# Kernel tuning notes

Measured on AMD Instinct MI355X. Metric: run time of the kernel, lower is better.

## Reference

```python
import jax, jax.numpy as jnp
import numpy as np

N_MET = 200000
N_RXN = 400000
E_SUB = 800000
E_ALL = 1600000
HIDDEN = 64
MSG = 8
DT = 0.01
FRAME = 100
PERIOD = 1000.0
CIRC_AMP = 0.5
HOMEO = 0.1
BASELINE = 1.0


def setup_inputs() -> dict:
    key = jax.random.key(0)
    ks = jax.random.split(key, 12)
    x = jax.random.uniform(ks[0], (N_MET, 8), dtype=jnp.float32)
    met_sub = jax.random.randint(ks[1], (E_SUB,), 0, N_MET, dtype=jnp.int32)
    rxn_sub = jax.random.randint(ks[2], (E_SUB,), 0, N_RXN, dtype=jnp.int32)
    sto_sub = jax.random.uniform(ks[3], (E_SUB,), dtype=jnp.float32, minval=0.5, maxval=2.0)
    met_all = jax.random.randint(ks[4], (E_ALL,), 0, N_MET, dtype=jnp.int32)
    rxn_all = jax.random.randint(ks[5], (E_ALL,), 0, N_RXN, dtype=jnp.int32)
    sto_all = jax.random.normal(ks[6], (E_ALL,), dtype=jnp.float32)
    sub_w1 = jax.random.normal(ks[7], (2, HIDDEN), dtype=jnp.float32) / np.sqrt(2.0)
    sub_b1 = jnp.zeros((HIDDEN,), jnp.float32)
    sub_w2 = jax.random.normal(ks[8], (HIDDEN, MSG), dtype=jnp.float32) / np.sqrt(HIDDEN)
    sub_b2 = jnp.zeros((MSG,), jnp.float32)
    rate_w1 = jax.random.normal(ks[9], (MSG, HIDDEN), dtype=jnp.float32) / np.sqrt(MSG)
    rate_b1 = jnp.zeros((HIDDEN,), jnp.float32)
    rate_w2 = jax.random.normal(ks[10], (HIDDEN, 1), dtype=jnp.float32) / np.sqrt(HIDDEN)
    rate_b2 = jnp.zeros((1,), jnp.float32)
    log_k = jax.random.uniform(ks[11], (N_RXN,), dtype=jnp.float32, minval=-3.0, maxval=-1.0)
    return {"x": x, "met_sub": met_sub, "rxn_sub": rxn_sub, "sto_sub": sto_sub,
            "met_all": met_all, "rxn_all": rxn_all, "sto_all": sto_all,
            "sub_w1": sub_w1, "sub_b1": sub_b1, "sub_w2": sub_w2, "sub_b2": sub_b2,
            "rate_w1": rate_w1, "rate_b1": rate_b1, "rate_w2": rate_w2, "rate_b2": rate_b2,
            "log_k": log_k}


def reference(x, met_sub, rxn_sub, sto_sub, met_all, rxn_all, sto_all,
              sub_w1, sub_b1, sub_w2, sub_b2,
              rate_w1, rate_b1, rate_w2, rate_b2, log_k):
    conc = x[:, 3]                      # [N_MET]
    ext = x[:, 4] * 2.0                 # [N_MET]
    # per-substrate-edge message MLP: [E_SUB,2] -> [E_SUB,MSG]
    msg_in = jnp.stack([conc[met_sub], sto_sub], axis=-1)
    msg = jnp.tanh(msg_in @ sub_w1 + sub_b1) @ sub_w2 + sub_b2
    # scatter-add edge messages into reactions
    h_rxn = jax.ops.segment_sum(msg, rxn_sub, num_segments=N_RXN)  # [N_RXN, MSG]
    k = jnp.power(10.0, log_k)
    base_v = (jnp.tanh(h_rxn @ rate_w1 + rate_b1) @ rate_w2 + rate_b2)[:, 0]  # [N_RXN]
    # multiplicative_substrate modulation: mean external input over substrates
    n_sub = jnp.maximum(
        jax.ops.segment_sum(jnp.ones((E_SUB,), jnp.float32), rxn_sub, num_segments=N_RXN), 1.0)
    ext_mean = jax.ops.segment_sum(ext[met_sub], rxn_sub, num_segments=N_RXN) / n_sub
    v = k * ext_mean * base_v
    # flux limit (dt > 0): no substrate over-consumed in one step
    consumption = sto_sub * v[rxn_sub] * DT
    total = jax.ops.segment_sum(consumption, met_sub, num_segments=N_MET)
    active = total > 1e-12
    met_scale = jnp.where(active,
                          jnp.minimum(conc / jnp.where(active, total, 1.0), 1.0),
                          1.0)
    rxn_scale = jnp.minimum(
        jax.ops.segment_min(met_scale[met_sub], rxn_sub, num_segments=N_RXN), 1.0)
    v = v * rxn_scale
    # scatter stoichiometric contributions to metabolites
    contrib = sto_all * v[rxn_all]
    dxdt = jax.ops.segment_sum(contrib, met_all, num_segments=N_MET)
    # homeostatic relaxation with circadian-modulated constant baseline
    phase = 2.0 * np.pi * FRAME / PERIOD
    modulation = 1.0 + CIRC_AMP * np.sin(phase)
    c_target = BASELINE * modulation
    dxdt = dxdt - HOMEO * (conc - c_target)
    return dxdt[:, None]
```

## Files before the change

kernel.cpp:

```cpp
#include <hip/hip_runtime.h>

#define NMET 200000
#define NRXN 400000
#define ESUB 800000
#define EALL 1600000

#define NBB 196
#define EBA 8192
#define EBS 4096

#define NBUCK_M 391
#define NBUCK_R 782
#define MET_MASK 0x3FFFF
#define MCAP 1280

#define C_TARGET 1.29389262614623664f
#define DT_C 0.01f
#define HOMEO_C 0.1f
#define LOG2_10 3.32192809488736235f

__device__ __forceinline__ float fast_tanh(float x) {
    float e = __expf(2.0f * x);
    return 1.0f - 2.0f * __builtin_amdgcn_rcpf(e + 1.0f);
}

__global__ __launch_bounds__(512) void k_count_all(
    const int* __restrict__ met_all, const int* __restrict__ met_sub,
    const int* __restrict__ rxn_sub,
    int* __restrict__ blockHistA, int* __restrict__ blockHistS,
    int* __restrict__ blockHistR)
{
    __shared__ int hA[NBUCK_M];
    __shared__ int hS[NBUCK_M];
    __shared__ int hR[NBUCK_R];
    int t = threadIdx.x;
    for (int b = t; b < NBUCK_R; b += 512) hR[b] = 0;
    for (int b = t; b < NBUCK_M; b += 512) { hA[b] = 0; hS[b] = 0; }
    __syncthreads();
    int baseA = blockIdx.x * EBA;
    for (int i = t; i < EBA; i += 512) {
        int e = baseA + i;
        if (e < EALL) atomicAdd(&hA[met_all[e] >> 9], 1);
    }
    int baseS = blockIdx.x * EBS;
    for (int i = t; i < EBS; i += 512) {
        int e = baseS + i;
        if (e < ESUB) {
            atomicAdd(&hS[met_sub[e] >> 9], 1);
            atomicAdd(&hR[rxn_sub[e] >> 9], 1);
        }
    }
    __syncthreads();
    for (int b = t; b < NBUCK_M; b += 512) {
        blockHistA[(size_t)b * NBB + blockIdx.x] = hA[b];
        blockHistS[(size_t)b * NBB + blockIdx.x] = hS[b];
    }
    for (int b = t; b < NBUCK_R; b += 512)
        blockHistR[(size_t)b * NBB + blockIdx.x] = hR[b];
}

__global__ __launch_bounds__(256) void k_scan_all(
    int* __restrict__ blockHistA, int* __restrict__ blockHistS,
    int* __restrict__ blockHistR,
    int* __restrict__ btotalA, int* __restrict__ btotalS,
    int* __restrict__ btotalR)
{
    __shared__ int sc[256];
    int bid = blockIdx.x;
    int* row; int* tot;
    if (bid < NBUCK_M) { row = blockHistA + (size_t)bid * NBB; tot = btotalA + bid; }
    else if (bid < 2 * NBUCK_M) { row = blockHistS + (size_t)(bid - NBUCK_M) * NBB; tot = btotalS + (bid - NBUCK_M); }
    else { row = blockHistR + (size_t)(bid - 2 * NBUCK_M) * NBB; tot = btotalR + (bid - 2 * NBUCK_M); }
    int t = threadIdx.x;
    int val = (t < NBB) ? row[t] : 0;
    sc[t] = val;
    __syncthreads();
    for (int off = 1; off < 256; off <<= 1) {
        int add = (t >= off) ? sc[t - off] : 0;
        __syncthreads();
        sc[t] += add;
        __syncthreads();
    }
    if (t < NBB) row[t] = sc[t] - val;
    if (t == 255) *tot = sc[255];
}

__global__ __launch_bounds__(1024) void k_bstart3(
    const int* __restrict__ btotalA, int* __restrict__ startA,
    const int* __restrict__ btotalS, int* __restrict__ startS,
    const int* __restrict__ btotalR, int* __restrict__ startR)
{
    __shared__ int lds[1024];
    const int* tot; int* st; int nb;
    if (blockIdx.x == 0)      { tot = btotalA; st = startA; nb = NBUCK_M; }
    else if (blockIdx.x == 1) { tot = btotalS; st = startS; nb = NBUCK_M; }
    else                      { tot = btotalR; st = startR; nb = NBUCK_R; }
    int t = threadIdx.x;
    int val = (t < nb) ? tot[t] : 0;
    lds[t] = val;
    __syncthreads();
    for (int off = 1; off < 1024; off <<= 1) {
        int add = (t >= off) ? lds[t - off] : 0;
        __syncthreads();
        lds[t] += add;
        __syncthreads();
    }
    if (t < nb) st[t] = lds[t] - val;
    if (t == 1023) st[nb] = lds[1023];
}

__global__ __launch_bounds__(512) void k_rxn_scatter(
    const int* __restrict__ rxn_sub, const int* __restrict__ met_sub,
    const float* __restrict__ sto_sub,
    const int* __restrict__ blockHistR, const int* __restrict__ bucketStartR,
    uint2* __restrict__ recsR)
{
    __shared__ int cnt[NBUCK_R];
    __shared__ int loff[NBUCK_R];
    __shared__ int rnk[NBUCK_R];
    __shared__ int bbase[NBUCK_R];
    __shared__ unsigned short sbuck[EBS];
    __shared__ uint2 stage[EBS];
    __shared__ int sc[512];
    __shared__ int carry_s;
    int t = threadIdx.x;
    for (int b = t; b < NBUCK_R; b += 512) {
        cnt[b] = 0; rnk[b] = 0;
        bbase[b] = bucketStartR[b] + blockHistR[(size_t)b * NBB + blockIdx.x];
    }
    if (t == 0) carry_s = 0;
    __syncthreads();
    int base = blockIdx.x * EBS;
    int nrec = ESUB - base; if (nrec > EBS) nrec = EBS; if (nrec < 0) nrec = 0;

    for (int i = t; i < nrec; i += 512)
        atomicAdd(&cnt[rxn_sub[base + i] >> 9], 1);
    __syncthreads();
    for (int b0 = 0; b0 < NBUCK_R; b0 += 512) {
        int idx = b0 + t;
        int val = (idx < NBUCK_R) ? cnt[idx] : 0;
        sc[t] = val;
        __syncthreads();
        for (int off = 1; off < 512; off <<= 1) {
            int add = (t >= off) ? sc[t - off] : 0;
            __syncthreads();
            sc[t] += add;
            __syncthreads();
        }
        if (idx < NBUCK_R) loff[idx] = carry_s + sc[t] - val;
        __syncthreads();
        if (t == 511) carry_s += sc[511];
        __syncthreads();
    }
    for (int i = t; i < nrec; i += 512) {
        int e = base + i;
        int r = rxn_sub[e];
        int b = r >> 9;
        int pos = loff[b] + atomicAdd(&rnk[b], 1);
        uint2 rec;
        rec.x = (unsigned)(met_sub[e] | ((r & 511) << 18));
        rec.y = __float_as_uint(sto_sub[e]);
        stage[pos] = rec;
        sbuck[pos] = (unsigned short)b;
    }
    __syncthreads();
    for (int j = t; j < nrec; j += 512) {
        int b = sbuck[j];
        recsR[bbase[b] + (j - loff[b])] = stage[j];
    }
}

__global__ __launch_bounds__(256) void k_csr_bucket(
    const uint2* __restrict__ recsR, const int* __restrict__ bucketStartR,
    int* __restrict__ cntG, int* __restrict__ offG, uint2* __restrict__ recsC)
{
    __shared__ int cnt[512];
    __shared__ int loff[512];
    __shared__ int pscan[256];
    __shared__ int rnk[512];
    int t = threadIdx.x;
    cnt[t] = 0; cnt[t + 256] = 0;
    rnk[t] = 0; rnk[t + 256] = 0;
    __syncthreads();

    int b = blockIdx.x;
    int s = bucketStartR[b], epos = bucketStartR[b + 1];
    for (int i = s + t; i < epos; i += 256)
        atomicAdd(&cnt[(recsR[i].x >> 18) & 511], 1);
    __syncthreads();

    int c0 = cnt[2 * t], c1 = cnt[2 * t + 1];
    int ps = c0 + c1;
    pscan[t] = ps;
    __syncthreads();
    for (int off = 1; off < 256; off <<= 1) {
        int add = (t >= off) ? pscan[t - off] : 0;
        __syncthreads();
        pscan[t] += add;
        __syncthreads();
    }
    int excl = pscan[t] - ps;
    loff[2 * t] = excl;
    loff[2 * t + 1] = excl + c0;
    __syncthreads();

    int gb = b << 9;
    for (int j = t; j < 512; j += 256) {
        cntG[gb + j] = cnt[j];
        offG[gb + j] = s + loff[j];
    }

    for (int i = s + t; i < epos; i += 256) {
        uint2 rec = recsR[i];
        int rloc = (rec.x >> 18) & 511;
        int pos = loff[rloc] + atomicAdd(&rnk[rloc], 1);
        recsC[s + pos] = rec;
    }
}

__global__ __launch_bounds__(512) void k_bucket2(
    const uint2* __restrict__ recsC, const int* __restrict__ bucketStartR,
    const int* __restrict__ cntG, const int* __restrict__ offG,
    const float* __restrict__ x,
    const float* __restrict__ sub_w1, const float* __restrict__ sub_b1,
    const float* __restrict__ sub_w2, const float* __restrict__ sub_b2,
    const float* __restrict__ rate_w1, const float* __restrict__ rate_b1,
    const float* __restrict__ rate_w2, const float* __restrict__ rate_b2,
    const float* __restrict__ log_k, float* __restrict__ v)
{
    __shared__ float sW1[128];
    __shared__ float sB1[64];
    __shared__ __align__(16) float sW2[512];
    __shared__ __align__(16) float sR1[512];
    __shared__ float sRB1[64];
    __shared__ float sR2[64];
    __shared__ float sB2[8];
    __shared__ float sRB2;
    __shared__ float msgL[MCAP][9];
    int t = threadIdx.x;
    sW2[t] = sub_w2[t];
    sR1[t] = rate_w1[t];
    if (t < 128) sW1[t] = sub_w1[t];
    if (t < 64) { sB1[t] = sub_b1[t]; sRB1[t] = rate_b1[t]; sR2[t] = rate_w2[t]; }
    if (t < 8) sB2[t] = sub_b2[t];
    if (t == 8) sRB2 = rate_b2[0];
    __syncthreads();

    int b = blockIdx.x;
    int s = bucketStartR[b], epos = bucketStartR[b + 1];
    int gr = (b << 9) + t;
    int n = cntG[gr];
    int base = offG[gr];
    float fn = (float)n;
    float h0 = fn * sB2[0], h1 = fn * sB2[1], h2 = fn * sB2[2], h3 = fn * sB2[3];
    float h4 = fn * sB2[4], h5 = fn * sB2[5], h6 = fn * sB2[6], h7 = fn * sB2[7];
    float exs = 0.f;

    for (int cb = s; cb < epos; cb += MCAP) {
        int ce = epos; if (ce > cb + MCAP) ce = cb + MCAP;
        for (int i = cb + t; i < ce; i += 512) {
            uint2 rec = recsC[i];
            int m = rec.x & MET_MASK;
            float st = __uint_as_float(rec.y);
            float c  = x[(size_t)m * 8 + 3];
            float ex = x[(size_t)m * 8 + 4];
            float m0 = 0.f, m1 = 0.f, m2 = 0.f, m3 = 0.f;
            float m4 = 0.f, m5 = 0.f, m6 = 0.f, m7 = 0.f;
            #pragma unroll 8
            for (int j = 0; j < 64; ++j) {
                float z = fmaf(c, sW1[j], fmaf(st, sW1[64 + j], sB1[j]));
                float th = fast_tanh(z);
                float4 wa = *(const float4*)&sW2[j * 8];
                float4 wb = *(const float4*)&sW2[j * 8 + 4];
                m0 = fmaf(th, wa.x, m0); m1 = fmaf(th, wa.y, m1);
                m2 = fmaf(th, wa.z, m2); m3 = fmaf(th, wa.w, m3);
                m4 = fmaf(th, wb.x, m4); m5 = fmaf(th, wb.y, m5);
                m6 = fmaf(th, wb.z, m6); m7 = fmaf(th, wb.w, m7);
            }
            float* row = msgL[i - cb];
            row[0] = m0; row[1] = m1; row[2] = m2; row[3] = m3;
            row[4] = m4; row[5] = m5; row[6] = m6; row[7] = m7;
            row[8] = ex;
        }
        __syncthreads();
        int lo = base;         if (lo < cb) lo = cb;
        int hi = base + n;     if (hi > ce) hi = ce;
        for (int k = lo; k < hi; ++k) {
            float* row = msgL[k - cb];
            h0 += row[0]; h1 += row[1]; h2 += row[2]; h3 += row[3];
            h4 += row[4]; h5 += row[5]; h6 += row[6]; h7 += row[7];
            exs += row[8];
        }
        __syncthreads();
    }

    if (gr < NRXN) {
        float acc = sRB2;
        #pragma unroll 4
        for (int j = 0; j < 64; ++j) {
            float z = sRB1[j];
            z = fmaf(h0, sR1[j],       z);
            z = fmaf(h1, sR1[64 + j],  z);
            z = fmaf(h2, sR1[128 + j], z);
            z = fmaf(h3, sR1[192 + j], z);
            z = fmaf(h4, sR1[256 + j], z);
            z = fmaf(h5, sR1[320 + j], z);
            z = fmaf(h6, sR1[384 + j], z);
            z = fmaf(h7, sR1[448 + j], z);
            acc = fmaf(fast_tanh(z), sR2[j], acc);
        }
        float nmax = fmaxf(fn, 1.0f);
        float ext_mean = 2.0f * exs * __builtin_amdgcn_rcpf(nmax);
        float kk = exp2f(log_k[gr] * LOG2_10);
        v[gr] = kk * ext_mean * acc;
    }
}

__global__ __launch_bounds__(512) void k_cons_scatter(
    const int* __restrict__ met_sub, const int* __restrict__ rxn_sub,
    const float* __restrict__ sto_sub, const float* __restrict__ v,
    const int* __restrict__ blockHistS, const int* __restrict__ bucketStartS,
    uint2* __restrict__ recsS)
{
    __shared__ int cnt[NBUCK_M];
    __shared__ int loff[NBUCK_M];
    __shared__ int rnk[NBUCK_M];
    __shared__ int bbase[NBUCK_M];
    __shared__ int sc[512];
    __shared__ uint2 stage[EBS];
    int t = threadIdx.x;
    for (int b = t; b < NBUCK_M; b += 512) {
        cnt[b] = 0; rnk[b] = 0;
        bbase[b] = bucketStartS[b] + blockHistS[(size_t)b * NBB + blockIdx.x];
    }
    __syncthreads();
    int base = blockIdx.x * EBS;
    int nrec = ESUB - base; if (nrec > EBS) nrec = EBS; if (nrec < 0) nrec = 0;

    for (int i = t; i < nrec; i += 512)
        atomicAdd(&cnt[met_sub[base + i] >> 9], 1);
    __syncthreads();
    int cval = (t < NBUCK_M) ? cnt[t] : 0;
    sc[t] = cval;
    __syncthreads();
    for (int off = 1; off < 512; off <<= 1) {
        int add = (t >= off) ? sc[t - off] : 0;
        __syncthreads();
        sc[t] += add;
        __syncthreads();
    }
    if (t < NBUCK_M) loff[t] = sc[t] - cval;
    __syncthreads();
    for (int i = t; i < nrec; i += 512) {
        int e = base + i;
        int m = met_sub[e];
        int b = m >> 9;
        float val = sto_sub[e] * v[rxn_sub[e]] * DT_C;
        int pos = loff[b] + atomicAdd(&rnk[b], 1);
        uint2 rec;
        rec.x = (unsigned)m;
        rec.y = __float_as_uint(val);
        stage[pos] = rec;
    }
    __syncthreads();
    for (int j = t; j < nrec; j += 512) {
        uint2 rec = stage[j];
        int b = (int)(rec.x >> 9);
        recsS[bbase[b] + (j - loff[b])] = rec;
    }
}

__global__ __launch_bounds__(512) void k_baccum_tot(
    const uint2* __restrict__ recsS, const int* __restrict__ bucketStartS,
    const float* __restrict__ x, float* __restrict__ met_scale)
{
    __shared__ float acc[512];
    int b = blockIdx.x;
    int t = threadIdx.x;
    acc[t] = 0.f;
    __syncthreads();
    int s = bucketStartS[b], epos = bucketStartS[b + 1];
    for (int i = s + t; i < epos; i += 512) {
        uint2 rec = recsS[i];
        atomicAdd(&acc[rec.x & 511], __uint_as_float(rec.y));
    }
    __syncthreads();
    int m = (b << 9) + t;
    if (m < NMET) {
        float tot = acc[t];
        float ms = 1.0f;
        if (tot > 1e-12f) ms = fminf(x[(size_t)m * 8 + 3] / tot, 1.0f);
        met_scale[m] = ms;
    }
}

__global__ __launch_bounds__(256) void k_rscale(
    const int* __restrict__ cntG, const int* __restrict__ offG,
    const uint2* __restrict__ recsC, const float* __restrict__ met_scale,
    float* __restrict__ v)
{
    int r = blockIdx.x * 256 + threadIdx.x;
    if (r >= NRXN) return;
    int n = cntG[r];
    int base = offG[r];
    float ms = 1.0f;
    for (int i = 0; i < n; ++i)
        ms = fminf(ms, met_scale[recsC[base + i].x & MET_MASK]);
    v[r] *= ms;
}

__global__ __launch_bounds__(512) void k_bscatter(
    const int* __restrict__ met_all, const int* __restrict__ rxn_all,
    const float* __restrict__ sto_all, const float* __restrict__ v,
    const int* __restrict__ blockHistA, const int* __restrict__ bucketStartA,
    uint2* __restrict__ recsA)
{
    __shared__ int cnt[NBUCK_M];
    __shared__ int loff[NBUCK_M];
    __shared__ int rnk[NBUCK_M];
    __shared__ int bbase[NBUCK_M];
    __shared__ int sc[512];
    __shared__ uint2 stage[EBA];
    int t = threadIdx.x;
    for (int b = t; b < NBUCK_M; b += 512) {
        cnt[b] = 0; rnk[b] = 0;
        bbase[b] = bucketStartA[b] + blockHistA[(size_t)b * NBB + blockIdx.x];
    }
    __syncthreads();
    int base = blockIdx.x * EBA;
    int nrec = EALL - base; if (nrec > EBA) nrec = EBA; if (nrec < 0) nrec = 0;

    for (int i = t; i < nrec; i += 512)
        atomicAdd(&cnt[met_all[base + i] >> 9], 1);
    __syncthreads();
    int cval = (t < NBUCK_M) ? cnt[t] : 0;
    sc[t] = cval;
    __syncthreads();
    for (int off = 1; off < 512; off <<= 1) {
        int add = (t >= off) ? sc[t - off] : 0;
        __syncthreads();
        sc[t] += add;
        __syncthreads();
    }
    if (t < NBUCK_M) loff[t] = sc[t] - cval;
    __syncthreads();
    for (int i = t; i < nrec; i += 512) {
        int e = base + i;
        int m = met_all[e];
        int b = m >> 9;
        float val = sto_all[e] * v[rxn_all[e]];
        int pos = loff[b] + atomicAdd(&rnk[b], 1);
        uint2 rec;
        rec.x = (unsigned)m;
        rec.y = __float_as_uint(val);
        stage[pos] = rec;
    }
    __syncthreads();
    for (int j = t; j < nrec; j += 512) {
        uint2 rec = stage[j];
        int b = (int)(rec.x >> 9);
        recsA[bbase[b] + (j - loff[b])] = rec;
    }
}

__global__ __launch_bounds__(512) void k_baccum(
    const uint2* __restrict__ recsA, const int* __restrict__ bucketStartA,
    const float* __restrict__ x, float* __restrict__ out)
{
    __shared__ float acc[512];
    int b = blockIdx.x;
    int t = threadIdx.x;
    acc[t] = 0.f;
    __syncthreads();
    int s = bucketStartA[b], epos = bucketStartA[b + 1];
    for (int i = s + t; i < epos; i += 512) {
        uint2 rec = recsA[i];
        atomicAdd(&acc[rec.x & 511], __uint_as_float(rec.y));
    }
    __syncthreads();
    int m = (b << 9) + t;
    if (m < NMET) {
        float c = x[(size_t)m * 8 + 3];
        out[m] = acc[t] - HOMEO_C * (c - C_TARGET);
    }
}

extern "C" void kernel_launch(void* const* d_in, const int* in_sizes, int n_in,
                              void* d_out, int out_size, void* d_ws, size_t ws_size,
                              hipStream_t stream) {
    const float* x       = (const float*)d_in[0];
    const int*   met_sub = (const int*)  d_in[1];
    const int*   rxn_sub = (const int*)  d_in[2];
    const float* sto_sub = (const float*)d_in[3];
    const int*   met_all = (const int*)  d_in[4];
    const int*   rxn_all = (const int*)  d_in[5];
    const float* sto_all = (const float*)d_in[6];
    const float* sub_w1  = (const float*)d_in[7];
    const float* sub_b1  = (const float*)d_in[8];
    const float* sub_w2  = (const float*)d_in[9];
    const float* sub_b2  = (const float*)d_in[10];
    const float* rate_w1 = (const float*)d_in[11];
    const float* rate_b1 = (const float*)d_in[12];
    const float* rate_w2 = (const float*)d_in[13];
    const float* rate_b2 = (const float*)d_in[14];
    const float* log_k   = (const float*)d_in[15];

    char* ws = (char*)d_ws;
    uint2* recsR = (uint2*)ws;
    uint2* recsC = recsR + ESUB;
    uint2* recsS = recsC + ESUB;
    uint2* recsA = recsS + ESUB;
    float* v     = (float*)(recsA + EALL);
    float* met_scale = v + NRXN;
    int* cntG = (int*)(met_scale + NMET);
    int* offG = cntG + (size_t)NBUCK_R * 512;
    int* blockHistA = offG + (size_t)NBUCK_R * 512;
    int* blockHistS = blockHistA + (size_t)NBUCK_M * NBB;
    int* blockHistR = blockHistS + (size_t)NBUCK_M * NBB;
    int* btotalA = blockHistR + (size_t)NBUCK_R * NBB;
    int* bucketStartA = btotalA + NBUCK_M;
    int* btotalS = bucketStartA + NBUCK_M + 1;
    int* bucketStartS = btotalS + NBUCK_M;
    int* btotalR = bucketStartS + NBUCK_M + 1;
    int* bucketStartR = btotalR + NBUCK_R;
    float* out = (float*)d_out;

    dim3 blk256(256);
    dim3 blk512(512);
    k_count_all<<<dim3(NBB), blk512, 0, stream>>>(
        met_all, met_sub, rxn_sub, blockHistA, blockHistS, blockHistR);
    k_scan_all<<<dim3(2 * NBUCK_M + NBUCK_R), blk256, 0, stream>>>(
        blockHistA, blockHistS, blockHistR, btotalA, btotalS, btotalR);
    k_bstart3<<<dim3(3), dim3(1024), 0, stream>>>(
        btotalA, bucketStartA, btotalS, bucketStartS, btotalR, bucketStartR);
    k_rxn_scatter<<<dim3(NBB), blk512, 0, stream>>>(
        rxn_sub, met_sub, sto_sub, blockHistR, bucketStartR, recsR);
    k_csr_bucket<<<dim3(NBUCK_R), blk256, 0, stream>>>(
        recsR, bucketStartR, cntG, offG, recsC);
    k_bucket2<<<dim3(NBUCK_R), blk512, 0, stream>>>(
        recsC, bucketStartR, cntG, offG, x,
        sub_w1, sub_b1, sub_w2, sub_b2,
        rate_w1, rate_b1, rate_w2, rate_b2, log_k, v);
    k_cons_scatter<<<dim3(NBB), blk512, 0, stream>>>(
        met_sub, rxn_sub, sto_sub, v, blockHistS, bucketStartS, recsS);
    k_baccum_tot<<<dim3(NBUCK_M), blk512, 0, stream>>>(
        recsS, bucketStartS, x, met_scale);
    k_rscale<<<dim3((NRXN + 255) / 256), blk256, 0, stream>>>(
        cntG, offG, recsC, met_scale, v);
    k_bscatter<<<dim3(NBB), blk512, 0, stream>>>(
        met_all, rxn_all, sto_all, v, blockHistA, bucketStartA, recsA);
    k_baccum<<<dim3(NBUCK_M), blk512, 0, stream>>>(recsA, bucketStartA, x, out);
}
```

Before: 162.3 us.

## Pack x gathers into widened reaction records and halve scatter block size

The substrate-edge records become 16 bytes and carry conc and ext values, gathered from x during the reaction scatter. This removes the random x gathers from the MLP bucket kernel. The scatter now stages a 16-bit permutation in LDS instead of full records and re-reads the inputs in sorted order. The edge blocks are halved and the block count doubled, with the histogram scan widened to 512 threads. In exchange, the record traffic through the two sort passes doubles, and the scatter kernel now does the random x gathers and re-reads its inputs.

```diff
diff --git a/kernel.cpp b/kernel.cpp
--- a/kernel.cpp
+++ b/kernel.cpp
@@ -5,9 +5,9 @@
 #define ESUB 800000
 #define EALL 1600000
 
-#define NBB 196
-#define EBA 8192
-#define EBS 4096
+#define NBB 392
+#define EBA 4096
+#define EBS 2048
 
 #define NBUCK_M 391
 #define NBUCK_R 782
@@ -59,13 +59,13 @@
         blockHistR[(size_t)b * NBB + blockIdx.x] = hR[b];
 }
 
-__global__ __launch_bounds__(256) void k_scan_all(
+__global__ __launch_bounds__(512) void k_scan_all(
     int* __restrict__ blockHistA, int* __restrict__ blockHistS,
     int* __restrict__ blockHistR,
     int* __restrict__ btotalA, int* __restrict__ btotalS,
     int* __restrict__ btotalR)
 {
-    __shared__ int sc[256];
+    __shared__ int sc[512];
     int bid = blockIdx.x;
     int* row; int* tot;
     if (bid < NBUCK_M) { row = blockHistA + (size_t)bid * NBB; tot = btotalA + bid; }
@@ -75,14 +75,14 @@
     int val = (t < NBB) ? row[t] : 0;
     sc[t] = val;
     __syncthreads();
-    for (int off = 1; off < 256; off <<= 1) {
+    for (int off = 1; off < 512; off <<= 1) {
         int add = (t >= off) ? sc[t - off] : 0;
         __syncthreads();
         sc[t] += add;
         __syncthreads();
     }
     if (t < NBB) row[t] = sc[t] - val;
-    if (t == 255) *tot = sc[255];
+    if (t == 511) *tot = sc[511];
 }
 
 __global__ __launch_bounds__(1024) void k_bstart3(
@@ -111,18 +111,18 @@
 
 __global__ __launch_bounds__(512) void k_rxn_scatter(
     const int* __restrict__ rxn_sub, const int* __restrict__ met_sub,
-    const float* __restrict__ sto_sub,
+    const float* __restrict__ sto_sub, const float* __restrict__ x,
     const int* __restrict__ blockHistR, const int* __restrict__ bucketStartR,
-    uint2* __restrict__ recsR)
+    uint4* __restrict__ recsR)
 {
     __shared__ int cnt[NBUCK_R];
     __shared__ int loff[NBUCK_R];
     __shared__ int rnk[NBUCK_R];
     __shared__ int bbase[NBUCK_R];
-    __shared__ unsigned short sbuck[EBS];
-    __shared__ uint2 stage[EBS];
     __shared__ int sc[512];
     __shared__ int carry_s;
+    __shared__ unsigned short perm[EBS];
+    __shared__ unsigned short sbuck[EBS];
     int t = threadIdx.x;
     for (int b = t; b < NBUCK_R; b += 512) {
         cnt[b] = 0; rnk[b] = 0;
@@ -153,26 +153,29 @@
         __syncthreads();
     }
     for (int i = t; i < nrec; i += 512) {
-        int e = base + i;
-        int r = rxn_sub[e];
-        int b = r >> 9;
+        int b = rxn_sub[base + i] >> 9;
         int pos = loff[b] + atomicAdd(&rnk[b], 1);
-        uint2 rec;
-        rec.x = (unsigned)(met_sub[e] | ((r & 511) << 18));
-        rec.y = __float_as_uint(sto_sub[e]);
-        stage[pos] = rec;
+        perm[pos] = (unsigned short)i;
         sbuck[pos] = (unsigned short)b;
     }
     __syncthreads();
     for (int j = t; j < nrec; j += 512) {
         int b = sbuck[j];
-        recsR[bbase[b] + (j - loff[b])] = stage[j];
+        int e = base + perm[j];
+        int r = rxn_sub[e];
+        int m = met_sub[e];
+        uint4 rec;
+        rec.x = (unsigned)(m | ((r & 511) << 18));
+        rec.y = __float_as_uint(sto_sub[e]);
+        rec.z = __float_as_uint(x[(size_t)m * 8 + 3]);
+        rec.w = __float_as_uint(x[(size_t)m * 8 + 4]);
+        recsR[bbase[b] + (j - loff[b])] = rec;
     }
 }
 
 __global__ __launch_bounds__(256) void k_csr_bucket(
-    const uint2* __restrict__ recsR, const int* __restrict__ bucketStartR,
-    int* __restrict__ cntG, int* __restrict__ offG, uint2* __restrict__ recsC)
+    const uint4* __restrict__ recsR, const int* __restrict__ bucketStartR,
+    int* __restrict__ cntG, int* __restrict__ offG, uint4* __restrict__ recsC)
 {
     __shared__ int cnt[512];
     __shared__ int loff[512];
@@ -211,7 +214,7 @@
     }
 
     for (int i = s + t; i < epos; i += 256) {
-        uint2 rec = recsR[i];
+        uint4 rec = recsR[i];
         int rloc = (rec.x >> 18) & 511;
         int pos = loff[rloc] + atomicAdd(&rnk[rloc], 1);
         recsC[s + pos] = rec;
@@ -219,9 +222,8 @@
 }
 
 __global__ __launch_bounds__(512) void k_bucket2(
-    const uint2* __restrict__ recsC, const int* __restrict__ bucketStartR,
+    const uint4* __restrict__ recsC, const int* __restrict__ bucketStartR,
     const int* __restrict__ cntG, const int* __restrict__ offG,
-    const float* __restrict__ x,
     const float* __restrict__ sub_w1, const float* __restrict__ sub_b1,
     const float* __restrict__ sub_w2, const float* __restrict__ sub_b2,
     const float* __restrict__ rate_w1, const float* __restrict__ rate_b1,
@@ -259,11 +261,10 @@
     for (int cb = s; cb < epos; cb += MCAP) {
         int ce = epos; if (ce > cb + MCAP) ce = cb + MCAP;
         for (int i = cb + t; i < ce; i += 512) {
-            uint2 rec = recsC[i];
-            int m = rec.x & MET_MASK;
+            uint4 rec = recsC[i];
             float st = __uint_as_float(rec.y);
-            float c  = x[(size_t)m * 8 + 3];
-            float ex = x[(size_t)m * 8 + 4];
+            float c  = __uint_as_float(rec.z);
+            float ex = __uint_as_float(rec.w);
             float m0 = 0.f, m1 = 0.f, m2 = 0.f, m3 = 0.f;
             float m4 = 0.f, m5 = 0.f, m6 = 0.f, m7 = 0.f;
             #pragma unroll 8
@@ -396,7 +397,7 @@
 
 __global__ __launch_bounds__(256) void k_rscale(
     const int* __restrict__ cntG, const int* __restrict__ offG,
-    const uint2* __restrict__ recsC, const float* __restrict__ met_scale,
+    const uint4* __restrict__ recsC, const float* __restrict__ met_scale,
     float* __restrict__ v)
 {
     int r = blockIdx.x * 256 + threadIdx.x;
@@ -506,9 +507,9 @@
     const float* log_k   = (const float*)d_in[15];
 
     char* ws = (char*)d_ws;
-    uint2* recsR = (uint2*)ws;
-    uint2* recsC = recsR + ESUB;
-    uint2* recsS = recsC + ESUB;
+    uint4* recsR = (uint4*)ws;
+    uint4* recsC = recsR + ESUB;
+    uint2* recsS = (uint2*)(recsC + ESUB);
     uint2* recsA = recsS + ESUB;
     float* v     = (float*)(recsA + EALL);
     float* met_scale = v + NRXN;
@@ -529,16 +530,16 @@
     dim3 blk512(512);
     k_count_all<<<dim3(NBB), blk512, 0, stream>>>(
         met_all, met_sub, rxn_sub, blockHistA, blockHistS, blockHistR);
-    k_scan_all<<<dim3(2 * NBUCK_M + NBUCK_R), blk256, 0, stream>>>(
+    k_scan_all<<<dim3(2 * NBUCK_M + NBUCK_R), blk512, 0, stream>>>(
         blockHistA, blockHistS, blockHistR, btotalA, btotalS, btotalR);
     k_bstart3<<<dim3(3), dim3(1024), 0, stream>>>(
         btotalA, bucketStartA, btotalS, bucketStartS, btotalR, bucketStartR);
     k_rxn_scatter<<<dim3(NBB), blk512, 0, stream>>>(
-        rxn_sub, met_sub, sto_sub, blockHistR, bucketStartR, recsR);
+        rxn_sub, met_sub, sto_sub, x, blockHistR, bucketStartR, recsR);
     k_csr_bucket<<<dim3(NBUCK_R), blk256, 0, stream>>>(
         recsR, bucketStartR, cntG, offG, recsC);
     k_bucket2<<<dim3(NBUCK_R), blk512, 0, stream>>>(
-        recsC, bucketStartR, cntG, offG, x,
+        recsC, bucketStartR, cntG, offG,
         sub_w1, sub_b1, sub_w2, sub_b2,
         rate_w1, rate_b1, rate_w2, rate_b2, log_k, v);
     k_cons_scatter<<<dim3(NBB), blk512, 0, stream>>>(
```

After: 172.8 us. 6.5% more time.
